# Performance work log

Hardware: AMD Instinct MI355X
Metric: run time of the kernel (lower is better)

The kernel has to match this reference:

```python
import jax, jax.numpy as jnp
import numpy as np
import math

L = 16.0
DT = 1.0
TAU = 10.0
THRESHOLD = 1.0
ALPHA = 0.01
DECAY = math.exp(-DT / TAU)

@jax.custom_vjp
def multibit_spike(x):
    # forward: floor(x) clipped to [0, L]
    return jnp.clip(jnp.floor(x), 0.0, L)

def _spike_fwd(x):
    return multibit_spike(x), x

def _spike_bwd(x, g):
    dist = jnp.abs(x - jnp.round(x))
    scale = jnp.clip(1.0 - 2.0 * dist, 0.0, 1.0)
    in_range = ((x >= 0.0) & (x <= L + 1.0)).astype(g.dtype)
    return (g * in_range * scale,)

multibit_spike.defvjp(_spike_fwd, _spike_bwd)

def setup_inputs() -> dict:
    key = jax.random.key(0)
    k_x, k_w = jax.random.split(key)
    B, T, IN, H = 16, 2048, 512, 512
    # SNN-aware init: std = 0.5*threshold / (sqrt(fan_in)*0.3)
    std = 0.5 * THRESHOLD / (math.sqrt(IN) * 0.3)
    x = jax.random.normal(k_x, (B, T, IN), dtype=jnp.float32)
    W = jax.random.normal(k_w, (H, IN), dtype=jnp.float32) * std
    b = jnp.zeros((H,), dtype=jnp.float32)
    return {"x": x, "W": W, "b": b}

def reference(x, W, b):
    B, T, _ = x.shape
    Hd = W.shape[0]
    # batched linear projection of the whole sequence (compute-heavy GEMM)
    h = jnp.einsum('bti,hi->bth', x, W) + b  # [B, T, H]
    v0 = jnp.zeros((B, Hd), dtype=x.dtype)
    theta0 = jnp.full((B, Hd), THRESHOLD, dtype=x.dtype)

    def step(carry, i_t):
        v, theta = carry
        v = v * DECAY + i_t
        clamp_limit = L * theta * 2.0
        v = jnp.clip(v, -clamp_limit, clamp_limit)
        spike = multibit_spike(v / theta)
        v = v - spike * theta
        theta = theta + ALPHA * spike - ALPHA * (theta - THRESHOLD)
        return (v, theta), spike

    (v_f, theta_f), spikes_tbh = jax.lax.scan(step, (v0, theta0), jnp.swapaxes(h, 0, 1))
    spikes = jnp.swapaxes(spikes_tbh, 0, 1)  # [B, T, H]
    return spikes, v_f, theta_f
```

## Files before the change

kernel.cpp:

```cpp
#include <hip/hip_runtime.h>

#define B_  16
#define T_  2048
#define IN_ 512
#define H_  512
#define M_  (B_ * T_)

#define BM 128
#define BN 128
#define BK 16
#define LDT (BM + 4)

static __device__ __forceinline__ float4 ld4(const float* p) {
    return *reinterpret_cast<const float4*>(p);
}

__global__ __launch_bounds__(256)
void gemm_xwT(const float* __restrict__ X, const float* __restrict__ W,
              const float* __restrict__ bias, float* __restrict__ Hout) {
    __shared__ float As[BK][LDT];
    __shared__ float Bs[BK][LDT];

    const int tid = threadIdx.x;
    const int m0  = blockIdx.x * BM;
    const int n0  = blockIdx.y * BN;

    const int tx = tid & 15;
    const int ty = tid >> 4;

    const int row = tid >> 2;
    const int kph = (tid & 3) * 4;

    const float* pa0 = X + (size_t)(m0 + row) * IN_ + kph;
    const float* pa1 = pa0 + (size_t)64 * IN_;
    const float* pb0 = W + (size_t)(n0 + row) * IN_ + kph;
    const float* pb1 = pb0 + (size_t)64 * IN_;

    float4 ra0 = ld4(pa0), ra1 = ld4(pa1), rb0 = ld4(pb0), rb1 = ld4(pb1);

    float acc[8][8];
#pragma unroll
    for (int i = 0; i < 8; ++i)
#pragma unroll
        for (int j = 0; j < 8; ++j) acc[i][j] = 0.0f;

    for (int k0 = 0; k0 < IN_; k0 += BK) {
        As[kph + 0][row]      = ra0.x;  As[kph + 1][row]      = ra0.y;
        As[kph + 2][row]      = ra0.z;  As[kph + 3][row]      = ra0.w;
        As[kph + 0][row + 64] = ra1.x;  As[kph + 1][row + 64] = ra1.y;
        As[kph + 2][row + 64] = ra1.z;  As[kph + 3][row + 64] = ra1.w;
        Bs[kph + 0][row]      = rb0.x;  Bs[kph + 1][row]      = rb0.y;
        Bs[kph + 2][row]      = rb0.z;  Bs[kph + 3][row]      = rb0.w;
        Bs[kph + 0][row + 64] = rb1.x;  Bs[kph + 1][row + 64] = rb1.y;
        Bs[kph + 2][row + 64] = rb1.z;  Bs[kph + 3][row + 64] = rb1.w;
        __syncthreads();

        if (k0 + BK < IN_) {
            ra0 = ld4(pa0 + k0 + BK);  ra1 = ld4(pa1 + k0 + BK);
            rb0 = ld4(pb0 + k0 + BK);  rb1 = ld4(pb1 + k0 + BK);
        }

#pragma unroll
        for (int k = 0; k < BK; ++k) {
            float4 av0 = ld4(&As[k][ty * 4]);
            float4 av1 = ld4(&As[k][ty * 4 + 64]);
            float4 bv0 = ld4(&Bs[k][tx * 4]);
            float4 bv1 = ld4(&Bs[k][tx * 4 + 64]);
            const float am[8] = {av0.x, av0.y, av0.z, av0.w,
                                 av1.x, av1.y, av1.z, av1.w};
            const float bn8[8] = {bv0.x, bv0.y, bv0.z, bv0.w,
                                  bv1.x, bv1.y, bv1.z, bv1.w};
#pragma unroll
            for (int i = 0; i < 8; ++i)
#pragma unroll
                for (int j = 0; j < 8; ++j)
                    acc[i][j] = fmaf(am[i], bn8[j], acc[i][j]);
        }
        __syncthreads();
    }

    float4 bb0 = ld4(&bias[n0 + tx * 4]);
    float4 bb1 = ld4(&bias[n0 + tx * 4 + 64]);
#pragma unroll
    for (int i = 0; i < 8; ++i) {
        const int r = m0 + ((i < 4) ? (ty * 4 + i) : (64 + ty * 4 + (i - 4)));
        float4 o0, o1;
        o0.x = acc[i][0] + bb0.x;  o0.y = acc[i][1] + bb0.y;
        o0.z = acc[i][2] + bb0.z;  o0.w = acc[i][3] + bb0.w;
        o1.x = acc[i][4] + bb1.x;  o1.y = acc[i][5] + bb1.y;
        o1.z = acc[i][6] + bb1.z;  o1.w = acc[i][7] + bb1.w;
        *reinterpret_cast<float4*>(&Hout[(size_t)r * H_ + n0 + tx * 4])      = o0;
        *reinterpret_cast<float4*>(&Hout[(size_t)r * H_ + n0 + tx * 4 + 64]) = o1;
    }
}

#define SPF 32

__device__ __forceinline__
void scan_steps(const float* __restrict__ buf, float* __restrict__ sp,
                int tb, float& v, float& theta) {
    const float DECAY_F = 0.9048374180359595f;
    const float ALPHA_F = 0.01f;
#pragma unroll
    for (int j = 0; j < SPF; ++j) {
        float cur = buf[j];
        v = v * DECAY_F + cur;
        float cl = 32.0f * theta;
        v = __builtin_amdgcn_fmed3f(v, -cl, cl);

        float r0 = __builtin_amdgcn_rcpf(theta);
        float e0 = fmaf(-theta, r0, 1.0f);
        float r1 = fmaf(r0, e0, r0);
        float q0 = v * r1;
        float er = fmaf(-theta, q0, v);
        float q  = fmaf(er, r1, q0);

        float s = floorf(q);
        s = __builtin_amdgcn_fmed3f(s, 0.0f, 16.0f);
        v = v - s * theta;
        theta = theta + ALPHA_F * s - ALPHA_F * (theta - 1.0f);
        sp[(size_t)(tb + j) * H_] = s;
    }
}

__global__ __launch_bounds__(64)
void gif_scan(const float* __restrict__ Hbuf, float* __restrict__ spikes,
              float* __restrict__ vout, float* __restrict__ thout) {
    const int gid = blockIdx.x * 64 + threadIdx.x;
    const int b = gid >> 9;
    const int h = gid & 511;

    const float* ip = Hbuf   + (size_t)b * T_ * H_ + h;
    float*       sp = spikes + (size_t)b * T_ * H_ + h;

    float bufA[SPF], bufB[SPF];
#pragma unroll
    for (int j = 0; j < SPF; ++j) bufA[j] = ip[(size_t)j * H_];

    float v = 0.0f, theta = 1.0f;
    for (int t0 = 0; t0 < T_; t0 += 2 * SPF) {
#pragma unroll
        for (int j = 0; j < SPF; ++j) bufB[j] = ip[(size_t)(t0 + SPF + j) * H_];
        asm volatile("" ::: "memory");
        scan_steps(bufA, sp, t0, v, theta);

        if (t0 + 2 * SPF < T_) {
#pragma unroll
            for (int j = 0; j < SPF; ++j)
                bufA[j] = ip[(size_t)(t0 + 2 * SPF + j) * H_];
        }
        asm volatile("" ::: "memory");
        scan_steps(bufB, sp, t0 + SPF, v, theta);
    }
    vout[gid]  = v;
    thout[gid] = theta;
}

extern "C" void kernel_launch(void* const* d_in, const int* in_sizes, int n_in,
                              void* d_out, int out_size, void* d_ws, size_t ws_size,
                              hipStream_t stream) {
    const float* x    = (const float*)d_in[0];
    const float* W    = (const float*)d_in[1];
    const float* bias = (const float*)d_in[2];

    float* out    = (float*)d_out;
    float* spikes = out;
    float* v_f    = out + (size_t)M_ * H_;
    float* th_f   = v_f + (size_t)B_ * H_;

    float* hbuf   = (float*)d_ws;

    dim3 grid(M_ / BM, H_ / BN);
    gemm_xwT<<<grid, 256, 0, stream>>>(x, W, bias, hbuf);
    gif_scan<<<(B_ * H_) / 64, 64, 0, stream>>>(hbuf, spikes, v_f, th_f);
}
```

Measured before the change: 370.2 us.

## Double-buffer GEMM shared tiles and speculatively precompute threshold reciprocal in scan

```diff
diff --git a/kernel.cpp b/kernel.cpp
--- a/kernel.cpp
+++ b/kernel.cpp
@@ -18,8 +18,8 @@
 __global__ __launch_bounds__(256)
 void gemm_xwT(const float* __restrict__ X, const float* __restrict__ W,
               const float* __restrict__ bias, float* __restrict__ Hout) {
-    __shared__ float As[BK][LDT];
-    __shared__ float Bs[BK][LDT];
+    __shared__ float As[2][BK][LDT];
+    __shared__ float Bs[2][BK][LDT];
 
     const int tid = threadIdx.x;
     const int m0  = blockIdx.x * BM;
@@ -44,15 +44,20 @@
 #pragma unroll
         for (int j = 0; j < 8; ++j) acc[i][j] = 0.0f;
 
+    int bsel = 0;
+#pragma unroll 1
     for (int k0 = 0; k0 < IN_; k0 += BK) {
-        As[kph + 0][row]      = ra0.x;  As[kph + 1][row]      = ra0.y;
-        As[kph + 2][row]      = ra0.z;  As[kph + 3][row]      = ra0.w;
-        As[kph + 0][row + 64] = ra1.x;  As[kph + 1][row + 64] = ra1.y;
-        As[kph + 2][row + 64] = ra1.z;  As[kph + 3][row + 64] = ra1.w;
-        Bs[kph + 0][row]      = rb0.x;  Bs[kph + 1][row]      = rb0.y;
-        Bs[kph + 2][row]      = rb0.z;  Bs[kph + 3][row]      = rb0.w;
-        Bs[kph + 0][row + 64] = rb1.x;  Bs[kph + 1][row + 64] = rb1.y;
-        Bs[kph + 2][row + 64] = rb1.z;  Bs[kph + 3][row + 64] = rb1.w;
+        float (*__restrict__ Asb)[LDT] = As[bsel];
+        float (*__restrict__ Bsb)[LDT] = Bs[bsel];
+
+        Asb[kph + 0][row]      = ra0.x;  Asb[kph + 1][row]      = ra0.y;
+        Asb[kph + 2][row]      = ra0.z;  Asb[kph + 3][row]      = ra0.w;
+        Asb[kph + 0][row + 64] = ra1.x;  Asb[kph + 1][row + 64] = ra1.y;
+        Asb[kph + 2][row + 64] = ra1.z;  Asb[kph + 3][row + 64] = ra1.w;
+        Bsb[kph + 0][row]      = rb0.x;  Bsb[kph + 1][row]      = rb0.y;
+        Bsb[kph + 2][row]      = rb0.z;  Bsb[kph + 3][row]      = rb0.w;
+        Bsb[kph + 0][row + 64] = rb1.x;  Bsb[kph + 1][row + 64] = rb1.y;
+        Bsb[kph + 2][row + 64] = rb1.z;  Bsb[kph + 3][row + 64] = rb1.w;
         __syncthreads();
 
         if (k0 + BK < IN_) {
@@ -62,10 +67,10 @@
 
 #pragma unroll
         for (int k = 0; k < BK; ++k) {
-            float4 av0 = ld4(&As[k][ty * 4]);
-            float4 av1 = ld4(&As[k][ty * 4 + 64]);
-            float4 bv0 = ld4(&Bs[k][tx * 4]);
-            float4 bv1 = ld4(&Bs[k][tx * 4 + 64]);
+            float4 av0 = ld4(&Asb[k][ty * 4]);
+            float4 av1 = ld4(&Asb[k][ty * 4 + 64]);
+            float4 bv0 = ld4(&Bsb[k][tx * 4]);
+            float4 bv1 = ld4(&Bsb[k][tx * 4 + 64]);
             const float am[8] = {av0.x, av0.y, av0.z, av0.w,
                                  av1.x, av1.y, av1.z, av1.w};
             const float bn8[8] = {bv0.x, bv0.y, bv0.z, bv0.w,
@@ -76,7 +81,7 @@
                 for (int j = 0; j < 8; ++j)
                     acc[i][j] = fmaf(am[i], bn8[j], acc[i][j]);
         }
-        __syncthreads();
+        bsel ^= 1;
     }
 
     float4 bb0 = ld4(&bias[n0 + tx * 4]);
@@ -98,7 +103,7 @@
 
 __device__ __forceinline__
 void scan_steps(const float* __restrict__ buf, float* __restrict__ sp,
-                int tb, float& v, float& theta) {
+                int tb, float& v, float& theta, float& rp, float& s_prev) {
     const float DECAY_F = 0.9048374180359595f;
     const float ALPHA_F = 0.01f;
 #pragma unroll
@@ -108,17 +113,25 @@
         float cl = 32.0f * theta;
         v = __builtin_amdgcn_fmed3f(v, -cl, cl);
 
-        float r0 = __builtin_amdgcn_rcpf(theta);
-        float e0 = fmaf(-theta, r0, 1.0f);
-        float r1 = fmaf(r0, e0, r0);
-        float q0 = v * r1;
+        float dlt = fmaf(0.01f, s_prev, -0.08f);
+        float tcr = fmaf(-rp, dlt, 1.0f);
+        float rr  = rp * tcr;
+        float e;
+        e = fmaf(-theta, rr, 1.0f);  rr = fmaf(rr, e, rr);
+        e = fmaf(-theta, rr, 1.0f);  rr = fmaf(rr, e, rr);
+        e = fmaf(-theta, rr, 1.0f);  rr = fmaf(rr, e, rr);
+        float q0 = v * rr;
         float er = fmaf(-theta, q0, v);
-        float q  = fmaf(er, r1, q0);
+        float q  = fmaf(er, rr, q0);
 
         float s = floorf(q);
         s = __builtin_amdgcn_fmed3f(s, 0.0f, 16.0f);
         v = v - s * theta;
         theta = theta + ALPHA_F * s - ALPHA_F * (theta - 1.0f);
+
+        rp = __builtin_amdgcn_rcpf(fmaf(0.99f, theta, 0.09f));
+        s_prev = s;
+
         sp[(size_t)(tb + j) * H_] = s;
     }
 }
@@ -138,11 +151,14 @@
     for (int j = 0; j < SPF; ++j) bufA[j] = ip[(size_t)j * H_];
 
     float v = 0.0f, theta = 1.0f;
+    float rp = __builtin_amdgcn_rcpf(1.08f);
+    float s_prev = 0.0f;
+
     for (int t0 = 0; t0 < T_; t0 += 2 * SPF) {
 #pragma unroll
         for (int j = 0; j < SPF; ++j) bufB[j] = ip[(size_t)(t0 + SPF + j) * H_];
         asm volatile("" ::: "memory");
-        scan_steps(bufA, sp, t0, v, theta);
+        scan_steps(bufA, sp, t0, v, theta, rp, s_prev);
 
         if (t0 + 2 * SPF < T_) {
 #pragma unroll
@@ -150,7 +166,7 @@
                 bufA[j] = ip[(size_t)(t0 + 2 * SPF + j) * H_];
         }
         asm volatile("" ::: "memory");
-        scan_steps(bufB, sp, t0 + SPF, v, theta);
+        scan_steps(bufB, sp, t0 + SPF, v, theta, rp, s_prev);
     }
     vout[gid]  = v;
     thout[gid] = theta;
```

Measured after the change: 408.5 us. +10.3%, slower.
